# Kernel optimization log

Hardware: AMD Instinct MI355X
Metric: run time of the kernel (lower is better)

The kernel has to match this reference:

```python
import jax, jax.numpy as jnp
import numpy as np

T, B, E, H, V = 512, 512, 128, 64, 50001  # seq_len, batch, embed_dim, hidden, vocab(+unk)


def _gru_dir(x, h0, w_ih, w_hh, b_ih, b_hh):
    """Single-direction GRU (PyTorch gate math). x: [T,B,E], h0: [B,H] -> ([T,B,H], [B,H])."""
    xg = jnp.einsum('tbe,ge->tbg', x, w_ih) + b_ih  # [T,B,3H], one big GEMM

    def step(h, xg_t):
        hg = h @ w_hh.T + b_hh  # [B,3H]
        xr, xz, xn = jnp.split(xg_t, 3, axis=-1)
        hr, hz, hn = jnp.split(hg, 3, axis=-1)
        r = jax.nn.sigmoid(xr + hr)
        z = jax.nn.sigmoid(xz + hz)
        n = jnp.tanh(xn + r * hn)
        h_new = (1.0 - z) * n + z * h
        return h_new, h_new

    h_last, hs = jax.lax.scan(step, h0, xg)
    return hs, h_last


def setup_inputs() -> dict:
    key = jax.random.key(0)
    ks = jax.random.split(key, 14)
    s = 0.05  # matches _create_weights(mean=0, std=0.05)
    g = 1.0 / np.sqrt(H)  # torch GRU default init scale
    f32 = jnp.float32
    return {
        'input': jax.random.randint(ks[0], (T, B), 0, V),
        'hidden_state': jnp.zeros((2, B, H), f32),
        'embed': jax.random.normal(ks[1], (V, E), f32),
        'word_weight': jax.random.normal(ks[2], (2 * H, 2 * H), f32) * s,
        'word_bias': jax.random.normal(ks[3], (1, 2 * H), f32) * s,
        'context_weight': jax.random.normal(ks[4], (2 * H, 1), f32) * s,
        'w_ih_f': jax.random.normal(ks[5], (3 * H, E), f32) * g,
        'w_hh_f': jax.random.normal(ks[6], (3 * H, H), f32) * g,
        'b_ih_f': jax.random.normal(ks[7], (3 * H,), f32) * g,
        'b_hh_f': jax.random.normal(ks[8], (3 * H,), f32) * g,
        'w_ih_b': jax.random.normal(ks[9], (3 * H, E), f32) * g,
        'w_hh_b': jax.random.normal(ks[10], (3 * H, H), f32) * g,
        'b_ih_b': jax.random.normal(ks[11], (3 * H,), f32) * g,
        'b_hh_b': jax.random.normal(ks[12], (3 * H,), f32) * g,
    }


def reference(input, hidden_state, embed, word_weight, word_bias, context_weight,
              w_ih_f, w_hh_f, b_ih_f, b_hh_f, w_ih_b, w_hh_b, b_ih_b, b_hh_b):
    x = embed[input]  # [T,B,E]
    hs_f, hT_f = _gru_dir(x, hidden_state[0], w_ih_f, w_hh_f, b_ih_f, b_hh_f)
    hs_b, hT_b = _gru_dir(x[::-1], hidden_state[1], w_ih_b, w_hh_b, b_ih_b, b_hh_b)
    h_t = jnp.concatenate([hs_f, hs_b[::-1]], axis=-1)  # [T,B,2H]
    h_n = jnp.stack([hT_f, hT_b], axis=0)               # [2,B,H]

    # attention: u_t = tanh(h_t @ W + b) batched over all timesteps at once
    u_t = jnp.tanh(jnp.einsum('tbh,hk->tbk', h_t, word_weight) + word_bias)  # [T,B,2H]
    scores = jnp.einsum('tbk,ko->tb', u_t, context_weight)                   # [T,B]
    a_t = jax.nn.softmax(scores, axis=0)  # softmax over time (dim=1 of [B,T])
    s_i = jnp.sum(h_t * a_t[:, :, None], axis=0, keepdims=True)  # [1,B,2H]
    return s_i, h_n
```

## Files before the change

kernel.cpp:

```cpp
#include <hip/hip_runtime.h>
#include <hip/hip_bf16.h>


#define T_LEN 512
#define B_SZ  512
#define E_DIM 128
#define H_DIM 64
#define G3    192
#define V_SZ  50001
#define TWOH  128

#define XGV_SZ (V_SZ * G3)
#define HS_SZ  (T_LEN * B_SZ * H_DIM)
#define OFF_XGV_F 0
#define OFF_XGV_B (XGV_SZ)
#define OFF_HS_F  (2 * XGV_SZ)
#define OFF_HS_B  (2 * XGV_SZ + HS_SZ)
#define OFF_SC    (2 * XGV_SZ + 2 * HS_SZ)

__device__ __forceinline__ float sigm(float x) {
    return 1.0f / (1.0f + __expf(-x));
}
__device__ __forceinline__ float tanh_fast(float x) {
    float ax = fminf(fabsf(x), 15.0f);
    float e  = __expf(2.0f * ax);
    float r  = 1.0f - 2.0f / (e + 1.0f);
    return copysignf(r, x);
}
__device__ __forceinline__ float rdlane_f(float v, int l) {
    return __uint_as_float(__builtin_amdgcn_readlane(__float_as_uint(v), l));
}
#define PIN(x) asm volatile("" : "+v"(x))

__global__ __launch_bounds__(256, 2) void xgv_kernel(
    const float* __restrict__ embed,
    const float* __restrict__ w_ih_f, const float* __restrict__ b_ih_f,
    const float* __restrict__ w_ih_b, const float* __restrict__ b_ih_b,
    float* __restrict__ ws)
{
    const int dir = blockIdx.y;
    const float* __restrict__ w_ih = dir ? w_ih_b : w_ih_f;
    const float* __restrict__ b_ih = dir ? b_ih_b : b_ih_f;
    float* __restrict__ xgv = ws + (dir ? OFF_XGV_B : OFF_XGV_F);
    const int v0 = blockIdx.x * 64;
    const int j  = threadIdx.x & 63;
    const int s  = threadIdx.x >> 6;

    float accr[16], accz[16], accn[16];
#pragma unroll
    for (int k = 0; k < 16; ++k) { accr[k] = 0.f; accz[k] = 0.f; accn[k] = 0.f; }

#pragma unroll 1
    for (int ec = 0; ec < 4; ++ec) {
        float wrc[32], wzc[32], wnc[32];
        const float4* wpr = (const float4*)(w_ih + (j      ) * 128 + ec * 32);
        const float4* wpz = (const float4*)(w_ih + (64  + j) * 128 + ec * 32);
        const float4* wpn = (const float4*)(w_ih + (128 + j) * 128 + ec * 32);
#pragma unroll
        for (int i = 0; i < 8; ++i) {
            float4 a = wpr[i];
            wrc[4*i+0] = a.x; wrc[4*i+1] = a.y; wrc[4*i+2] = a.z; wrc[4*i+3] = a.w;
            float4 b = wpz[i];
            wzc[4*i+0] = b.x; wzc[4*i+1] = b.y; wzc[4*i+2] = b.z; wzc[4*i+3] = b.w;
            float4 c = wpn[i];
            wnc[4*i+0] = c.x; wnc[4*i+1] = c.y; wnc[4*i+2] = c.z; wnc[4*i+3] = c.w;
        }
#pragma unroll
        for (int k = 0; k < 16; ++k) {
            const int v = v0 + s + 4 * k;
            if (v < V_SZ) {
                const float4* ep = (const float4*)(embed + v * 128 + ec * 32);
#pragma unroll
                for (int i = 0; i < 8; ++i) {
                    float4 e4 = ep[i];
                    accr[k] = fmaf(e4.x, wrc[4*i+0], accr[k]);
                    accr[k] = fmaf(e4.y, wrc[4*i+1], accr[k]);
                    accr[k] = fmaf(e4.z, wrc[4*i+2], accr[k]);
                    accr[k] = fmaf(e4.w, wrc[4*i+3], accr[k]);
                    accz[k] = fmaf(e4.x, wzc[4*i+0], accz[k]);
                    accz[k] = fmaf(e4.y, wzc[4*i+1], accz[k]);
                    accz[k] = fmaf(e4.z, wzc[4*i+2], accz[k]);
                    accz[k] = fmaf(e4.w, wzc[4*i+3], accz[k]);
                    accn[k] = fmaf(e4.x, wnc[4*i+0], accn[k]);
                    accn[k] = fmaf(e4.y, wnc[4*i+1], accn[k]);
                    accn[k] = fmaf(e4.z, wnc[4*i+2], accn[k]);
                    accn[k] = fmaf(e4.w, wnc[4*i+3], accn[k]);
                }
            }
        }
    }
    const float br = b_ih[j], bz = b_ih[64 + j], bn = b_ih[128 + j];
#pragma unroll
    for (int k = 0; k < 16; ++k) {
        const int v = v0 + s + 4 * k;
        if (v < V_SZ) {
            float* o = xgv + (size_t)v * G3;
            o[j]        = accr[k] + br;
            o[64 + j]   = accz[k] + bz;
            o[128 + j]  = accn[k] + bn;
        }
    }
}

#define GRU_STEP(hh)                                        \
    {                                                       \
        const float h0v = rdlane_f(h, (hh));                \
        const float h1v = rdlane_f(h, (hh) + 1);            \
        ar0 = fmaf(h0v, wr[(hh)],     ar0);                 \
        az0 = fmaf(h0v, wz[(hh)],     az0);                 \
        an0 = fmaf(h0v, wn[(hh)],     an0);                 \
        ar1 = fmaf(h1v, wr[(hh) + 1], ar1);                 \
        az1 = fmaf(h1v, wz[(hh) + 1], az1);                 \
        an1 = fmaf(h1v, wn[(hh) + 1], an1);                 \
    }

__global__ __launch_bounds__(64) __attribute__((amdgpu_waves_per_eu(1, 1)))
void gru_scan_kernel(
    const int*   __restrict__ input,
    const float* __restrict__ h0,
    const float* __restrict__ w_hh_f, const float* __restrict__ b_hh_f,
    const float* __restrict__ w_hh_b, const float* __restrict__ b_hh_b,
    float* __restrict__ ws, float* __restrict__ d_out)
{
    const int dir = blockIdx.y;
    const int j   = threadIdx.x & 63;
    const int b   = blockIdx.x;

    const float* __restrict__ w_hh = dir ? w_hh_b : w_hh_f;
    const float* __restrict__ b_hh = dir ? b_hh_b : b_hh_f;
    const float* __restrict__ xgv  = ws + (dir ? OFF_XGV_B : OFF_XGV_F);
    float* __restrict__ hs = ws + (dir ? OFF_HS_B : OFF_HS_F);

    float wr[64], wz[64], wn[64];
    {
        const float4* pr = (const float4*)(w_hh + (j      ) * 64);
        const float4* pz = (const float4*)(w_hh + (64  + j) * 64);
        const float4* pn = (const float4*)(w_hh + (128 + j) * 64);
#pragma unroll
        for (int i = 0; i < 16; ++i) {
            float4 a = pr[i];
            wr[4*i+0] = a.x; wr[4*i+1] = a.y; wr[4*i+2] = a.z; wr[4*i+3] = a.w;
            float4 bq = pz[i];
            wz[4*i+0] = bq.x; wz[4*i+1] = bq.y; wz[4*i+2] = bq.z; wz[4*i+3] = bq.w;
            float4 c = pn[i];
            wn[4*i+0] = c.x; wn[4*i+1] = c.y; wn[4*i+2] = c.z; wn[4*i+3] = c.w;
        }
    }
#pragma unroll
    for (int i = 0; i < 64; ++i) { PIN(wr[i]); PIN(wz[i]); PIN(wn[i]); }

    const float br = b_hh[j], bz = b_hh[64 + j], bn = b_hh[128 + j];

    float h = h0[dir * (B_SZ * H_DIM) + b * H_DIM + j];

    int tok0 = __builtin_amdgcn_readfirstlane(input[(dir ? (T_LEN - 1) : 0) * B_SZ + b]);
    int tok_next_raw = input[(dir ? (T_LEN - 2) : 1) * B_SZ + b];
    float xr = xgv[(size_t)tok0 * G3 + j];
    float xz = xgv[(size_t)tok0 * G3 + 64 + j];
    float xn = xgv[(size_t)tok0 * G3 + 128 + j];

    for (int t = 0; t < T_LEN; ++t) {
        int tok_pf_raw = 0;
        if (t + 2 < T_LEN) {
            const int te2 = dir ? (T_LEN - 3 - t) : (t + 2);
            tok_pf_raw = input[te2 * B_SZ + b];
        }
        float nxr = 0.f, nxz = 0.f, nxn = 0.f;
        if (t + 1 < T_LEN) {
            const int tn = __builtin_amdgcn_readfirstlane(tok_next_raw);
            nxr = xgv[(size_t)tn * G3 + j];
            nxz = xgv[(size_t)tn * G3 + 64 + j];
            nxn = xgv[(size_t)tn * G3 + 128 + j];
        }

        float ar0 = br,  az0 = bz,  an0 = bn;
        float ar1 = 0.f, az1 = 0.f, an1 = 0.f;
        GRU_STEP(0)  GRU_STEP(2)  GRU_STEP(4)  GRU_STEP(6)
        GRU_STEP(8)  GRU_STEP(10) GRU_STEP(12) GRU_STEP(14)
        GRU_STEP(16) GRU_STEP(18) GRU_STEP(20) GRU_STEP(22)
        GRU_STEP(24) GRU_STEP(26) GRU_STEP(28) GRU_STEP(30)
        GRU_STEP(32) GRU_STEP(34) GRU_STEP(36) GRU_STEP(38)
        GRU_STEP(40) GRU_STEP(42) GRU_STEP(44) GRU_STEP(46)
        GRU_STEP(48) GRU_STEP(50) GRU_STEP(52) GRU_STEP(54)
        GRU_STEP(56) GRU_STEP(58) GRU_STEP(60) GRU_STEP(62)
        const float hr = ar0 + ar1;
        const float hz = az0 + az1;
        const float hn = an0 + an1;

        const float rg = sigm(xr + hr);
        const float zg = sigm(xz + hz);
        const float ng = tanh_fast(xn + rg * hn);
        h = (1.0f - zg) * ng + zg * h;

        const int te = dir ? (T_LEN - 1 - t) : t;
        hs[(size_t)te * (B_SZ * H_DIM) + b * H_DIM + j] = h;

        xr = nxr; xz = nxz; xn = nxn;
        tok_next_raw = tok_pf_raw;
    }
    d_out[B_SZ * TWOH + dir * (B_SZ * H_DIM) + b * H_DIM + j] = h;
}

__global__ __launch_bounds__(256, 4) void attn_scores_kernel(
    const float* __restrict__ word_weight, const float* __restrict__ word_bias,
    const float* __restrict__ context_weight, float* __restrict__ ws)
{
    const int tid = threadIdx.x;
    const int l   = tid & 63;
    const int wv  = tid >> 6;
    const float* __restrict__ hs_f = ws + OFF_HS_F;
    const float* __restrict__ hs_b = ws + OFF_HS_B;
    float* __restrict__ sc = ws + OFF_SC;

    __shared__ float ht[64][129];
    __shared__ float part[4][64];

    const int r0 = blockIdx.x * 64;
    const int t  = r0 >> 9;
    const int b0 = r0 & 511;

    {
        const float* __restrict__ srcf = hs_f + (size_t)t * (B_SZ * H_DIM) + b0 * H_DIM;
        const float* __restrict__ srcb = hs_b + (size_t)t * (B_SZ * H_DIM) + b0 * H_DIM;
#pragma unroll
        for (int i = 0; i < 16; ++i) {
            const int idx = tid + i * 256;
            const int row = idx >> 6, hh = idx & 63;
            ht[row][hh]      = srcf[idx];
            ht[row][64 + hh] = srcb[idx];
        }
    }
    __syncthreads();

    const int k0 = __builtin_amdgcn_readfirstlane(wv * 32);

    float acc[32];
#pragma unroll
    for (int k = 0; k < 32; ++k) acc[k] = word_bias[k0 + k];

#pragma unroll 4
    for (int h = 0; h < 128; ++h) {
        const float hv = ht[l][h];
        const float* __restrict__ wrow = word_weight + h * 128 + k0;
#pragma unroll
        for (int k = 0; k < 32; ++k) acc[k] = fmaf(hv, wrow[k], acc[k]);
    }

    float p = 0.f;
#pragma unroll
    for (int k = 0; k < 32; ++k) p += tanh_fast(acc[k]) * context_weight[k0 + k];
    part[wv][l] = p;
    __syncthreads();

    if (wv == 0) {
        sc[(b0 + l) * T_LEN + t] =
            (part[0][l] + part[1][l]) + (part[2][l] + part[3][l]);
    }
}

__global__ __launch_bounds__(512, 2) void softmax_wsum_kernel(
    const float* __restrict__ ws_c, float* __restrict__ d_out)
{
    const float* __restrict__ hs_f = ws_c + OFF_HS_F;
    const float* __restrict__ hs_b = ws_c + OFF_HS_B;
    const float* __restrict__ sc   = ws_c + OFF_SC;
    const int b   = blockIdx.x;
    const int tid = threadIdx.x;

    __shared__ float red[8];
    __shared__ float sa[T_LEN];
    __shared__ float psum[4][TWOH];

    {
        const int t = tid;
        const int w = t >> 6;
        float v = sc[b * 512 + t];

        float m = v;
#pragma unroll
        for (int off = 32; off >= 1; off >>= 1) m = fmaxf(m, __shfl_xor(m, off));
        if ((t & 63) == 0) red[w] = m;
        __syncthreads();
        float mm = red[0];
#pragma unroll
        for (int i = 1; i < 8; ++i) mm = fmaxf(mm, red[i]);
        __syncthreads();

        const float e = __expf(v - mm);
        float ssum = e;
#pragma unroll
        for (int off = 32; off >= 1; off >>= 1) ssum += __shfl_xor(ssum, off);
        if ((t & 63) == 0) red[w] = ssum;
        __syncthreads();
        float tot = 0.f;
#pragma unroll
        for (int i = 0; i < 8; ++i) tot += red[i];

        sa[t] = e / tot;
    }
    __syncthreads();

    {
        const int k = tid & 127;
        const int c = tid >> 7;
        const float* __restrict__ src =
            ((k < 64) ? hs_f : hs_b) + (k & 63) + b * H_DIM;
        const int t0 = c * 128;

        float acc = 0.f, acc2 = 0.f;
#pragma unroll 8
        for (int t = 0; t < 128; t += 2) {
            acc  = fmaf(sa[t0 + t],     src[(size_t)(t0 + t)     * (B_SZ * H_DIM)], acc);
            acc2 = fmaf(sa[t0 + t + 1], src[(size_t)(t0 + t + 1) * (B_SZ * H_DIM)], acc2);
        }
        psum[c][k] = acc + acc2;
    }
    __syncthreads();
    if (tid < TWOH) {
        d_out[b * TWOH + tid] =
            (psum[0][tid] + psum[1][tid]) + (psum[2][tid] + psum[3][tid]);
    }
}

extern "C" void kernel_launch(void* const* d_in, const int* in_sizes, int n_in,
                              void* d_out, int out_size, void* d_ws, size_t ws_size,
                              hipStream_t stream)
{
    const int*   input  = (const int*)  d_in[0];
    const float* hidden = (const float*)d_in[1];
    const float* embed  = (const float*)d_in[2];
    const float* word_w = (const float*)d_in[3];
    const float* word_b = (const float*)d_in[4];
    const float* ctx_w  = (const float*)d_in[5];
    const float* w_ih_f = (const float*)d_in[6];
    const float* w_hh_f = (const float*)d_in[7];
    const float* b_ih_f = (const float*)d_in[8];
    const float* b_hh_f = (const float*)d_in[9];
    const float* w_ih_b = (const float*)d_in[10];
    const float* w_hh_b = (const float*)d_in[11];
    const float* b_ih_b = (const float*)d_in[12];
    const float* b_hh_b = (const float*)d_in[13];
    float* ws  = (float*)d_ws;
    float* out = (float*)d_out;

    xgv_kernel<<<dim3((V_SZ + 63) / 64, 2), 256, 0, stream>>>(
        embed, w_ih_f, b_ih_f, w_ih_b, b_ih_b, ws);
    gru_scan_kernel<<<dim3(B_SZ, 2), 64, 0, stream>>>(
        input, hidden, w_hh_f, b_hh_f, w_hh_b, b_hh_b, ws, out);
    attn_scores_kernel<<<(T_LEN * B_SZ) / 64, 256, 0, stream>>>(
        word_w, word_b, ctx_w, ws);
    softmax_wsum_kernel<<<B_SZ, 512, 0, stream>>>(ws, out);
}
```

Measured before the change: 797.6 us.

## Split GRU gates across three waves with LDS exchange of hidden state

```diff
diff --git a/kernel.cpp b/kernel.cpp
--- a/kernel.cpp
+++ b/kernel.cpp
@@ -27,10 +27,6 @@
     float r  = 1.0f - 2.0f / (e + 1.0f);
     return copysignf(r, x);
 }
-__device__ __forceinline__ float rdlane_f(float v, int l) {
-    return __uint_as_float(__builtin_amdgcn_readlane(__float_as_uint(v), l));
-}
-#define PIN(x) asm volatile("" : "+v"(x))
 
 __global__ __launch_bounds__(256, 2) void xgv_kernel(
     const float* __restrict__ embed,
@@ -102,19 +98,7 @@
     }
 }
 
-#define GRU_STEP(hh)                                        \
-    {                                                       \
-        const float h0v = rdlane_f(h, (hh));                \
-        const float h1v = rdlane_f(h, (hh) + 1);            \
-        ar0 = fmaf(h0v, wr[(hh)],     ar0);                 \
-        az0 = fmaf(h0v, wz[(hh)],     az0);                 \
-        an0 = fmaf(h0v, wn[(hh)],     an0);                 \
-        ar1 = fmaf(h1v, wr[(hh) + 1], ar1);                 \
-        az1 = fmaf(h1v, wz[(hh) + 1], az1);                 \
-        an1 = fmaf(h1v, wn[(hh) + 1], an1);                 \
-    }
-
-__global__ __launch_bounds__(64) __attribute__((amdgpu_waves_per_eu(1, 1)))
+__global__ __launch_bounds__(192, 2)
 void gru_scan_kernel(
     const int*   __restrict__ input,
     const float* __restrict__ h0,
@@ -123,7 +107,9 @@
     float* __restrict__ ws, float* __restrict__ d_out)
 {
     const int dir = blockIdx.y;
-    const int j   = threadIdx.x & 63;
+    const int tid = threadIdx.x;
+    const int j   = tid & 63;
+    const int g   = tid >> 6;
     const int b   = blockIdx.x;
 
     const float* __restrict__ w_hh = dir ? w_hh_b : w_hh_f;
@@ -131,33 +117,31 @@
     const float* __restrict__ xgv  = ws + (dir ? OFF_XGV_B : OFF_XGV_F);
     float* __restrict__ hs = ws + (dir ? OFF_HS_B : OFF_HS_F);
 
-    float wr[64], wz[64], wn[64];
+    __shared__ float h_l[64];
+    __shared__ float r_l[64];
+    __shared__ float z_l[64];
+    __shared__ float hn_l[64];
+
+    float w[64];
     {
-        const float4* pr = (const float4*)(w_hh + (j      ) * 64);
-        const float4* pz = (const float4*)(w_hh + (64  + j) * 64);
-        const float4* pn = (const float4*)(w_hh + (128 + j) * 64);
+        const float4* p = (const float4*)(w_hh + (g * 64 + j) * 64);
 #pragma unroll
         for (int i = 0; i < 16; ++i) {
-            float4 a = pr[i];
-            wr[4*i+0] = a.x; wr[4*i+1] = a.y; wr[4*i+2] = a.z; wr[4*i+3] = a.w;
-            float4 bq = pz[i];
-            wz[4*i+0] = bq.x; wz[4*i+1] = bq.y; wz[4*i+2] = bq.z; wz[4*i+3] = bq.w;
-            float4 c = pn[i];
-            wn[4*i+0] = c.x; wn[4*i+1] = c.y; wn[4*i+2] = c.z; wn[4*i+3] = c.w;
-        }
-    }
-#pragma unroll
-    for (int i = 0; i < 64; ++i) { PIN(wr[i]); PIN(wz[i]); PIN(wn[i]); }
-
-    const float br = b_hh[j], bz = b_hh[64 + j], bn = b_hh[128 + j];
-
-    float h = h0[dir * (B_SZ * H_DIM) + b * H_DIM + j];
+            float4 a = p[i];
+            w[4*i+0] = a.x; w[4*i+1] = a.y; w[4*i+2] = a.z; w[4*i+3] = a.w;
+        }
+    }
+    const float bg = b_hh[g * 64 + j];
+
+    float hprev = h0[dir * (B_SZ * H_DIM) + b * H_DIM + j];
+    if (g == 0) h_l[j] = hprev;
 
     int tok0 = __builtin_amdgcn_readfirstlane(input[(dir ? (T_LEN - 1) : 0) * B_SZ + b]);
     int tok_next_raw = input[(dir ? (T_LEN - 2) : 1) * B_SZ + b];
-    float xr = xgv[(size_t)tok0 * G3 + j];
-    float xz = xgv[(size_t)tok0 * G3 + 64 + j];
-    float xn = xgv[(size_t)tok0 * G3 + 128 + j];
+    float xg = xgv[(size_t)tok0 * G3 + g * 64 + j];
+    float xn = (g == 2) ? xg : xgv[(size_t)tok0 * G3 + 128 + j];
+
+    __syncthreads();
 
     for (int t = 0; t < T_LEN; ++t) {
         int tok_pf_raw = 0;
@@ -165,40 +149,46 @@
             const int te2 = dir ? (T_LEN - 3 - t) : (t + 2);
             tok_pf_raw = input[te2 * B_SZ + b];
         }
-        float nxr = 0.f, nxz = 0.f, nxn = 0.f;
+        float nxg = 0.f, nxn = 0.f;
         if (t + 1 < T_LEN) {
             const int tn = __builtin_amdgcn_readfirstlane(tok_next_raw);
-            nxr = xgv[(size_t)tn * G3 + j];
-            nxz = xgv[(size_t)tn * G3 + 64 + j];
-            nxn = xgv[(size_t)tn * G3 + 128 + j];
-        }
-
-        float ar0 = br,  az0 = bz,  an0 = bn;
-        float ar1 = 0.f, az1 = 0.f, an1 = 0.f;
-        GRU_STEP(0)  GRU_STEP(2)  GRU_STEP(4)  GRU_STEP(6)
-        GRU_STEP(8)  GRU_STEP(10) GRU_STEP(12) GRU_STEP(14)
-        GRU_STEP(16) GRU_STEP(18) GRU_STEP(20) GRU_STEP(22)
-        GRU_STEP(24) GRU_STEP(26) GRU_STEP(28) GRU_STEP(30)
-        GRU_STEP(32) GRU_STEP(34) GRU_STEP(36) GRU_STEP(38)
-        GRU_STEP(40) GRU_STEP(42) GRU_STEP(44) GRU_STEP(46)
-        GRU_STEP(48) GRU_STEP(50) GRU_STEP(52) GRU_STEP(54)
-        GRU_STEP(56) GRU_STEP(58) GRU_STEP(60) GRU_STEP(62)
-        const float hr = ar0 + ar1;
-        const float hz = az0 + az1;
-        const float hn = an0 + an1;
-
-        const float rg = sigm(xr + hr);
-        const float zg = sigm(xz + hz);
-        const float ng = tanh_fast(xn + rg * hn);
-        h = (1.0f - zg) * ng + zg * h;
-
-        const int te = dir ? (T_LEN - 1 - t) : t;
-        hs[(size_t)te * (B_SZ * H_DIM) + b * H_DIM + j] = h;
-
-        xr = nxr; xz = nxz; xn = nxn;
+            nxg = xgv[(size_t)tn * G3 + g * 64 + j];
+            nxn = (g == 2) ? nxg : xgv[(size_t)tn * G3 + 128 + j];
+        }
+
+        float a0 = bg, a1 = 0.f;
+#pragma unroll
+        for (int i = 0; i < 16; ++i) {
+            const float4 hv = *(const float4*)(h_l + 4 * i);
+            a0 = fmaf(hv.x, w[4*i+0], a0);
+            a1 = fmaf(hv.y, w[4*i+1], a1);
+            a0 = fmaf(hv.z, w[4*i+2], a0);
+            a1 = fmaf(hv.w, w[4*i+3], a1);
+        }
+        const float acc = a0 + a1;
+
+        if (g == 0)      r_l[j]  = sigm(xg + acc);
+        else if (g == 1) z_l[j]  = sigm(xg + acc);
+        else             hn_l[j] = acc;
+        __syncthreads();
+
+        const float rr = r_l[j], zz = z_l[j], hh = hn_l[j];
+        const float n    = tanh_fast(xn + rr * hh);
+        const float hnew = (1.0f - zz) * n + zz * hprev;
+        hprev = hnew;
+
+        if (g == 0) {
+            h_l[j] = hnew;
+            const int te = dir ? (T_LEN - 1 - t) : t;
+            hs[(size_t)te * (B_SZ * H_DIM) + b * H_DIM + j] = hnew;
+        }
+        __syncthreads();
+
+        xg = nxg; xn = nxn;
         tok_next_raw = tok_pf_raw;
     }
-    d_out[B_SZ * TWOH + dir * (B_SZ * H_DIM) + b * H_DIM + j] = h;
+    if (g == 0)
+        d_out[B_SZ * TWOH + dir * (B_SZ * H_DIM) + b * H_DIM + j] = hprev;
 }
 
 __global__ __launch_bounds__(256, 4) void attn_scores_kernel(
@@ -345,7 +335,7 @@
 
     xgv_kernel<<<dim3((V_SZ + 63) / 64, 2), 256, 0, stream>>>(
         embed, w_ih_f, b_ih_f, w_ih_b, b_ih_b, ws);
-    gru_scan_kernel<<<dim3(B_SZ, 2), 64, 0, stream>>>(
+    gru_scan_kernel<<<dim3(B_SZ, 2), 192, 0, stream>>>(
         input, hidden, w_hh_f, b_hh_f, w_hh_b, b_hh_b, ws, out);
     attn_scores_kernel<<<(T_LEN * B_SZ) / 64, 256, 0, stream>>>(
         word_w, word_b, ctx_w, ws);
```

New measurement: 1.012 ms. 1.27x slower.
